# Kernel tuning notes

Hardware: AMD Instinct MI355X
Metric: run time of the kernel (lower is better)

## Reference

```python
import jax, jax.numpy as jnp
import numpy as np

N_NODES = 50000
N_EDGES = 500000
D = 256  # node_dim = edge_dim = out_dim; in_dim = 2*D


def setup_inputs() -> dict:
    key = jax.random.key(0)
    ks = jax.random.split(key, 9)
    x = jax.random.normal(ks[0], (N_NODES, D), dtype=jnp.float32)
    edge_index = jax.random.randint(ks[1], (2, N_EDGES), 0, N_NODES, dtype=jnp.int64)
    edge_attr = jax.random.normal(ks[2], (N_EDGES, D), dtype=jnp.float32)
    u = jax.random.normal(ks[3], (1, D), dtype=jnp.float32)
    batch = jnp.zeros((N_NODES,), dtype=jnp.int64)
    scale = 1.0 / np.sqrt(2 * D)
    W1 = jax.random.normal(ks[4], (2 * D, D), dtype=jnp.float32) * scale
    b1 = jax.random.normal(ks[5], (D,), dtype=jnp.float32) * scale
    W2 = jax.random.normal(ks[6], (2 * D, D), dtype=jnp.float32) * scale
    b2 = jax.random.normal(ks[7], (D,), dtype=jnp.float32) * scale
    return {"x": x, "edge_index": edge_index, "edge_attr": edge_attr, "u": u,
            "batch": batch, "W1": W1, "b1": b1, "W2": W2, "b2": b2}


def reference(x, edge_index, edge_attr, u, batch, W1, b1, W2, b2):
    row, col = edge_index[0], edge_index[1]
    # gather source-node features and concat with edge features: [E, 2D]
    h = jnp.concatenate([x[row], edge_attr], axis=1)
    h = jax.nn.relu(h @ W1 + b1)  # node_mlp_1
    # scatter-mean over destination nodes
    agg = jax.ops.segment_sum(h, col, num_segments=N_NODES)
    cnt = jax.ops.segment_sum(jnp.ones((h.shape[0],), h.dtype), col, num_segments=N_NODES)
    agg = agg / jnp.maximum(cnt, 1.0)[:, None]
    out = jnp.concatenate([x, agg], axis=1)  # [N, 2D]
    return jax.nn.relu(out @ W2 + b2)  # node_mlp_2
```

## Files before the change

kernel.cpp:

```cpp
#include <hip/hip_runtime.h>

#define N_NODES 50000
#define N_EDGES 500000
#define D 256
#define TWO_D 512

typedef __attribute__((ext_vector_type(8))) __bf16 bf16x8;
typedef __attribute__((ext_vector_type(4))) float f32x4;
typedef unsigned short ushort_t;

__device__ __forceinline__ unsigned short f2bf(float f) {
    unsigned int u = __builtin_bit_cast(unsigned int, f);
    u += 0x7FFFu + ((u >> 16) & 1u);
    return (unsigned short)(u >> 16);
}
__device__ __forceinline__ unsigned int pk2(float lo, float hi) {
    return (unsigned int)f2bf(lo) | ((unsigned int)f2bf(hi) << 16);
}


__global__ void k_zero(float* __restrict__ p, int n4) {
    int i = blockIdx.x * blockDim.x + threadIdx.x;
    if (i < n4) ((float4*)p)[i] = make_float4(0.f, 0.f, 0.f, 0.f);
}

__global__ void k_cvt_x(const float* __restrict__ x, ushort_t* __restrict__ xb, int n8) {
    int i = blockIdx.x * blockDim.x + threadIdx.x;
    if (i < n8) {
        const float4* s = (const float4*)(x + (size_t)i * 8);
        float4 a = s[0], b = s[1];
        uint4 o;
        o.x = pk2(a.x, a.y); o.y = pk2(a.z, a.w);
        o.z = pk2(b.x, b.y); o.w = pk2(b.z, b.w);
        *(uint4*)(xb + (size_t)i * 8) = o;
    }
}

__global__ void k_wt(const float* __restrict__ w, ushort_t* __restrict__ wt, int KW) {
    int n = blockIdx.x;
    for (int k = threadIdx.x; k < KW; k += blockDim.x)
        wt[(size_t)n * KW + k] = f2bf(w[(size_t)k * D + n]);
}

__global__ void k_count_i(const int* __restrict__ coli, int* __restrict__ cnt) {
    int e = blockIdx.x * blockDim.x + threadIdx.x;
    if (e < N_EDGES) atomicAdd(&cnt[coli[e]], 1);
}


__device__ __forceinline__ int iscan_block(int v, int tid) {
    int lane = tid & 63, wv = tid >> 6;
    int s = v;
    #pragma unroll
    for (int off = 1; off < 64; off <<= 1) {
        int t = __shfl_up(s, off, 64);
        if (lane >= off) s += t;
    }
    __shared__ int wsum[4];
    if (lane == 63) wsum[wv] = s;
    __syncthreads();
    #pragma unroll
    for (int w = 0; w < 3; ++w)
        if (wv > w) s += wsum[w];
    return s;
}

__global__ void k_scan_a(const int* __restrict__ cnt, int* __restrict__ rowptr,
                         int* __restrict__ bsum) {
    int i = blockIdx.x * 256 + threadIdx.x;
    int v = (i < N_NODES) ? cnt[i] : 0;
    int s = iscan_block(v, threadIdx.x);
    if (i < N_NODES) rowptr[i] = s - v;
    if (threadIdx.x == 255) bsum[blockIdx.x] = s;
}

__global__ void k_scan_b(int* __restrict__ bsum, int nb) {
    int i = threadIdx.x;
    int v = (i < nb) ? bsum[i] : 0;
    int s = iscan_block(v, i);
    if (i < nb) bsum[i] = s - v;
}

__global__ void k_scan_c(int* __restrict__ rowptr, const int* __restrict__ bsum,
                         int* __restrict__ cursor) {
    int i = blockIdx.x * 256 + threadIdx.x;
    if (i < N_NODES) {
        int r = rowptr[i] + bsum[blockIdx.x];
        rowptr[i] = r;
        cursor[i] = r;
    }
    if (i == 0) rowptr[N_NODES] = N_EDGES;
}

__global__ void k_fill(const int* __restrict__ coli, const int* __restrict__ rowi,
                       int* __restrict__ cursor, int* __restrict__ elist,
                       int* __restrict__ rowg) {
    int e = blockIdx.x * blockDim.x + threadIdx.x;
    if (e < N_EDGES) {
        int p = atomicAdd(&cursor[coli[e]], 1);
        elist[p] = e;
        rowg[p] = rowi[e];
    }
}

__global__ void k_posnode(const int* __restrict__ rowptr, int* __restrict__ posnode) {
    int p = blockIdx.x * blockDim.x + threadIdx.x;
    if (p >= N_EDGES) return;
    int lo = 0, hi = N_NODES;
    while (hi - lo > 1) {
        int mid = (lo + hi) >> 1;
        if (rowptr[mid] <= p) lo = mid; else hi = mid;
    }
    posnode[p] = lo;
}

__global__ __launch_bounds__(256) void k_xw1(
    const ushort_t* __restrict__ xb, const ushort_t* __restrict__ w1at,
    const float* __restrict__ b1, float* __restrict__ xw1)
{
    __shared__ __align__(16) ushort_t As[64 * 64];
    __shared__ __align__(16) ushort_t Bs[256 * 64];
    const int tid = threadIdx.x;
    const int wave = tid >> 6, lane = tid & 63;
    const int lr = lane & 15, lh = lane >> 4;
    const int n0 = blockIdx.x * 64;

    const int sm = tid >> 2;
    const int sc = (tid & 3) << 4;
    int ns = n0 + sm; if (ns >= N_NODES) ns = N_NODES - 1;
    const ushort_t* xrow = xb + (size_t)ns * D;
    const ushort_t* wrow = w1at + (size_t)tid * D;
    const int swA = (sm & 7) << 3;
    const int swB = (tid & 7) << 3;

    f32x4 acc[4][4];
    #pragma unroll
    for (int i = 0; i < 4; ++i)
        #pragma unroll
        for (int j = 0; j < 4; ++j)
            acc[i][j] = (f32x4){0.f, 0.f, 0.f, 0.f};

    for (int kk = 0; kk < 4; ++kk) {
        const int k0 = kk << 6;
        const uint4* sx = (const uint4*)(xrow + k0 + sc);
        uint4 av0 = sx[0], av1 = sx[1];
        const uint4* wsv = (const uint4*)(wrow + k0);
        uint4 w0 = wsv[0], w1 = wsv[1], w2 = wsv[2], w3 = wsv[3];
        uint4 w4 = wsv[4], w5 = wsv[5], w6 = wsv[6], w7 = wsv[7];

        __syncthreads();
        *(uint4*)&As[sm * 64 + ( sc      ^ swA)] = av0;
        *(uint4*)&As[sm * 64 + ((sc + 8) ^ swA)] = av1;
        {
            const int base = tid * 64;
            *(uint4*)&Bs[base + ( 0 ^ swB)] = w0;
            *(uint4*)&Bs[base + ( 8 ^ swB)] = w1;
            *(uint4*)&Bs[base + (16 ^ swB)] = w2;
            *(uint4*)&Bs[base + (24 ^ swB)] = w3;
            *(uint4*)&Bs[base + (32 ^ swB)] = w4;
            *(uint4*)&Bs[base + (40 ^ swB)] = w5;
            *(uint4*)&Bs[base + (48 ^ swB)] = w6;
            *(uint4*)&Bs[base + (56 ^ swB)] = w7;
        }
        __syncthreads();

        #pragma unroll
        for (int kh = 0; kh < 2; ++kh) {
            const int kb = kh * 32 + lh * 8;
            bf16x8 af[4], bfr[4];
            #pragma unroll
            for (int i = 0; i < 4; ++i) {
                int m = i * 16 + lr;
                af[i] = *(const bf16x8*)&As[m * 64 + (kb ^ ((m & 7) << 3))];
            }
            #pragma unroll
            for (int j = 0; j < 4; ++j) {
                int n = wave * 64 + j * 16 + lr;
                bfr[j] = *(const bf16x8*)&Bs[n * 64 + (kb ^ ((n & 7) << 3))];
            }
            #pragma unroll
            for (int i = 0; i < 4; ++i)
                #pragma unroll
                for (int j = 0; j < 4; ++j)
                    acc[i][j] = __builtin_amdgcn_mfma_f32_16x16x32_bf16(af[i], bfr[j], acc[i][j], 0, 0, 0);
        }
    }

    float bv[4];
    #pragma unroll
    for (int j = 0; j < 4; ++j) bv[j] = b1[wave * 64 + j * 16 + lr];
    #pragma unroll
    for (int i = 0; i < 4; ++i) {
        #pragma unroll
        for (int r = 0; r < 4; ++r) {
            int m = i * 16 + lh * 4 + r;
            int node = n0 + m;
            if (node < N_NODES) {
                float* orow = xw1 + (size_t)node * D;
                #pragma unroll
                for (int j = 0; j < 4; ++j)
                    orow[wave * 64 + j * 16 + lr] = acc[i][j][r] + bv[j];
            }
        }
    }
}

__global__ __launch_bounds__(256, 3) void k_edge_csr(
    const float* __restrict__ ea, const ushort_t* __restrict__ w1bt,
    const float* __restrict__ xw1, const int* __restrict__ elist,
    const int* __restrict__ rowg, const int* __restrict__ posnode,
    const int* __restrict__ rowptr, float* __restrict__ agg)
{
    __shared__ __align__(16) ushort_t As[2][64 * 64];
    __shared__ int snd[64];
    const int tid = threadIdx.x;
    const int wave = tid >> 6, lane = tid & 63;
    const int lr = lane & 15, lh = lane >> 4;
    const int p0 = blockIdx.x * 64;

    if (tid < 64) {
        int p = p0 + tid;
        snd[tid] = (p < N_EDGES) ? posnode[min(p, N_EDGES - 1)] : -1;
    }

    const int sm = tid >> 2;
    const int sc = (tid & 3) << 4;
    int ps = p0 + sm; if (ps >= N_EDGES) ps = N_EDGES - 1;
    const float* earow = ea + (size_t)elist[ps] * D;
    const int swA = (sm & 7) << 3;

    const ushort_t* pw[4];
    #pragma unroll
    for (int j = 0; j < 4; ++j)
        pw[j] = w1bt + (size_t)(wave * 64 + j * 16 + lr) * D + lh * 8;

    f32x4 acc[4][4];
    #pragma unroll
    for (int i = 0; i < 4; ++i)
        #pragma unroll
        for (int j = 0; j < 4; ++j)
            acc[i][j] = (f32x4){0.f, 0.f, 0.f, 0.f};

    float4 a0, a1, a2, a3;
    {
        const float4* s = (const float4*)(earow + sc);
        a0 = s[0]; a1 = s[1]; a2 = s[2]; a3 = s[3];
    }
    {
        uint4 av0, av1;
        av0.x = pk2(a0.x, a0.y); av0.y = pk2(a0.z, a0.w);
        av0.z = pk2(a1.x, a1.y); av0.w = pk2(a1.z, a1.w);
        av1.x = pk2(a2.x, a2.y); av1.y = pk2(a2.z, a2.w);
        av1.z = pk2(a3.x, a3.y); av1.w = pk2(a3.z, a3.w);
        *(uint4*)&As[0][sm * 64 + ( sc      ^ swA)] = av0;
        *(uint4*)&As[0][sm * 64 + ((sc + 8) ^ swA)] = av1;
    }
    {
        const float4* s = (const float4*)(earow + 64 + sc);
        a0 = s[0]; a1 = s[1]; a2 = s[2]; a3 = s[3];
    }
    __syncthreads();

    #pragma unroll
    for (int kk = 0; kk < 4; ++kk) {
        const int k0 = kk << 6;
        const ushort_t* cur = As[kk & 1];

        bf16x8 b0[4], b1[4];
        #pragma unroll
        for (int j = 0; j < 4; ++j) {
            b0[j] = *(const bf16x8*)(pw[j] + k0);
            b1[j] = *(const bf16x8*)(pw[j] + k0 + 32);
        }
        bf16x8 af0[4], af1[4];
        #pragma unroll
        for (int i = 0; i < 4; ++i) {
            const int m = i * 16 + lr;
            const int sw = (m & 7) << 3;
            af0[i] = *(const bf16x8*)&cur[m * 64 + (( lh * 8      ) ^ sw)];
            af1[i] = *(const bf16x8*)&cur[m * 64 + ((32 + lh * 8) ^ sw)];
        }
        #pragma unroll
        for (int i = 0; i < 4; ++i)
            #pragma unroll
            for (int j = 0; j < 4; ++j) {
                acc[i][j] = __builtin_amdgcn_mfma_f32_16x16x32_bf16(af0[i], b0[j], acc[i][j], 0, 0, 0);
                acc[i][j] = __builtin_amdgcn_mfma_f32_16x16x32_bf16(af1[i], b1[j], acc[i][j], 0, 0, 0);
            }

        if (kk < 3) {
            uint4 av0, av1;
            av0.x = pk2(a0.x, a0.y); av0.y = pk2(a0.z, a0.w);
            av0.z = pk2(a1.x, a1.y); av0.w = pk2(a1.z, a1.w);
            av1.x = pk2(a2.x, a2.y); av1.y = pk2(a2.z, a2.w);
            av1.z = pk2(a3.x, a3.y); av1.w = pk2(a3.z, a3.w);
            ushort_t* nxt = (ushort_t*)As[(kk + 1) & 1];
            *(uint4*)&nxt[sm * 64 + ( sc      ^ swA)] = av0;
            *(uint4*)&nxt[sm * 64 + ((sc + 8) ^ swA)] = av1;
            if (kk < 2) {
                const float4* s = (const float4*)(earow + ((kk + 2) << 6) + sc);
                a0 = s[0]; a1 = s[1]; a2 = s[2]; a3 = s[3];
            }
            __syncthreads();
        }
    }

    #pragma unroll
    for (int i = 0; i < 4; ++i) {
        #pragma unroll
        for (int r = 0; r < 4; ++r) {
            const int m = i * 16 + lh * 4 + r;
            const bool ok = (p0 + m < N_EDGES);
            const int srw = rowg[min(p0 + m, N_EDGES - 1)];
            const float* xr = xw1 + (size_t)srw * D + wave * 64 + lr;
            #pragma unroll
            for (int j = 0; j < 4; ++j) {
                float v = acc[i][j][r] + xr[j * 16];
                v = v > 0.f ? v : 0.f;
                acc[i][j][r] = ok ? v : 0.f;
            }
        }
    }

    int a = 0;
    while (a < 64) {
        const int node = snd[a];
        int b = a + 1;
        while (b < 64 && snd[b] == node) ++b;
        if (node >= 0) {
            float s0 = 0.f, s1 = 0.f, s2 = 0.f, s3 = 0.f;
            #pragma unroll
            for (int i = 0; i < 4; ++i) {
                if (b <= i * 16 || a >= (i + 1) * 16) continue;
                #pragma unroll
                for (int r = 0; r < 4; ++r) {
                    const int m = i * 16 + lh * 4 + r;
                    const bool in = (m >= a) && (m < b);
                    s0 += in ? acc[i][0][r] : 0.f;
                    s1 += in ? acc[i][1][r] : 0.f;
                    s2 += in ? acc[i][2][r] : 0.f;
                    s3 += in ? acc[i][3][r] : 0.f;
                }
            }
            s0 += __shfl_xor(s0, 16, 64); s0 += __shfl_xor(s0, 32, 64);
            s1 += __shfl_xor(s1, 16, 64); s1 += __shfl_xor(s1, 32, 64);
            s2 += __shfl_xor(s2, 16, 64); s2 += __shfl_xor(s2, 32, 64);
            s3 += __shfl_xor(s3, 16, 64); s3 += __shfl_xor(s3, 32, 64);
            if (lh == 0) {
                const bool interior = (rowptr[node] >= p0) && (rowptr[node + 1] <= p0 + 64);
                float* dst = agg + (size_t)node * D + wave * 64 + lr;
                if (interior) {
                    dst[0]  = s0; dst[16] = s1; dst[32] = s2; dst[48] = s3;
                } else {
                    atomicAdd(&dst[0],  s0); atomicAdd(&dst[16], s1);
                    atomicAdd(&dst[32], s2); atomicAdd(&dst[48], s3);
                }
            }
        }
        a = b;
    }
}

__global__ __launch_bounds__(256) void k_node(
    const ushort_t* __restrict__ xb, const float* __restrict__ agg,
    const int* __restrict__ cnti,
    const ushort_t* __restrict__ w2t, const float* __restrict__ b2,
    float* __restrict__ out)
{
    __shared__ __align__(16) ushort_t As[64 * 64];
    __shared__ __align__(16) ushort_t Bs[256 * 64];
    const int tid = threadIdx.x;
    const int wave = tid >> 6, lane = tid & 63;
    const int lr = lane & 15, lh = lane >> 4;
    const int n0 = blockIdx.x * 64;

    const int sm = tid >> 2;
    const int sc = (tid & 3) << 4;
    int ns = n0 + sm; if (ns >= N_NODES) ns = N_NODES - 1;
    const ushort_t* xrow = xb + (size_t)ns * D;
    const float*    arow = agg + (size_t)ns * D;
    const float     ic   = 1.0f / fmaxf((float)cnti[ns], 1.0f);
    const ushort_t* wrow = w2t + (size_t)tid * TWO_D;
    const int swA = (sm & 7) << 3;
    const int swB = (tid & 7) << 3;

    f32x4 acc[4][4];
    #pragma unroll
    for (int i = 0; i < 4; ++i)
        #pragma unroll
        for (int j = 0; j < 4; ++j)
            acc[i][j] = (f32x4){0.f, 0.f, 0.f, 0.f};

    for (int kk = 0; kk < 8; ++kk) {
        const int k0 = kk << 6;
        uint4 av0, av1;
        if (kk < 4) {
            const uint4* s = (const uint4*)(xrow + k0 + sc);
            av0 = s[0]; av1 = s[1];
        } else {
            const float4* s = (const float4*)(arow + (k0 - D) + sc);
            float4 f0 = s[0], f1 = s[1], f2 = s[2], f3 = s[3];
            f0.x *= ic; f0.y *= ic; f0.z *= ic; f0.w *= ic;
            f1.x *= ic; f1.y *= ic; f1.z *= ic; f1.w *= ic;
            f2.x *= ic; f2.y *= ic; f2.z *= ic; f2.w *= ic;
            f3.x *= ic; f3.y *= ic; f3.z *= ic; f3.w *= ic;
            av0.x = pk2(f0.x, f0.y); av0.y = pk2(f0.z, f0.w);
            av0.z = pk2(f1.x, f1.y); av0.w = pk2(f1.z, f1.w);
            av1.x = pk2(f2.x, f2.y); av1.y = pk2(f2.z, f2.w);
            av1.z = pk2(f3.x, f3.y); av1.w = pk2(f3.z, f3.w);
        }
        const uint4* wsv = (const uint4*)(wrow + k0);
        uint4 w0 = wsv[0], w1 = wsv[1], w2 = wsv[2], w3 = wsv[3];
        uint4 w4 = wsv[4], w5 = wsv[5], w6 = wsv[6], w7 = wsv[7];

        __syncthreads();
        *(uint4*)&As[sm * 64 + ( sc      ^ swA)] = av0;
        *(uint4*)&As[sm * 64 + ((sc + 8) ^ swA)] = av1;
        {
            const int base = tid * 64;
            *(uint4*)&Bs[base + ( 0 ^ swB)] = w0;
            *(uint4*)&Bs[base + ( 8 ^ swB)] = w1;
            *(uint4*)&Bs[base + (16 ^ swB)] = w2;
            *(uint4*)&Bs[base + (24 ^ swB)] = w3;
            *(uint4*)&Bs[base + (32 ^ swB)] = w4;
            *(uint4*)&Bs[base + (40 ^ swB)] = w5;
            *(uint4*)&Bs[base + (48 ^ swB)] = w6;
            *(uint4*)&Bs[base + (56 ^ swB)] = w7;
        }
        __syncthreads();

        #pragma unroll
        for (int kh = 0; kh < 2; ++kh) {
            const int kb = kh * 32 + lh * 8;
            bf16x8 af[4], bfr[4];
            #pragma unroll
            for (int i = 0; i < 4; ++i) {
                int m = i * 16 + lr;
                af[i] = *(const bf16x8*)&As[m * 64 + (kb ^ ((m & 7) << 3))];
            }
            #pragma unroll
            for (int j = 0; j < 4; ++j) {
                int n = wave * 64 + j * 16 + lr;
                bfr[j] = *(const bf16x8*)&Bs[n * 64 + (kb ^ ((n & 7) << 3))];
            }
            #pragma unroll
            for (int i = 0; i < 4; ++i)
                #pragma unroll
                for (int j = 0; j < 4; ++j)
                    acc[i][j] = __builtin_amdgcn_mfma_f32_16x16x32_bf16(af[i], bfr[j], acc[i][j], 0, 0, 0);
        }
    }

    float bv[4];
    #pragma unroll
    for (int j = 0; j < 4; ++j) bv[j] = b2[wave * 64 + j * 16 + lr];
    #pragma unroll
    for (int i = 0; i < 4; ++i) {
        #pragma unroll
        for (int r = 0; r < 4; ++r) {
            int m = i * 16 + lh * 4 + r;
            int node = n0 + m;
            if (node < N_NODES) {
                float* orow = out + (size_t)node * D;
                #pragma unroll
                for (int j = 0; j < 4; ++j) {
                    float v = acc[i][j][r] + bv[j];
                    orow[wave * 64 + j * 16 + lr] = v > 0.f ? v : 0.f;
                }
            }
        }
    }
}


extern "C" void kernel_launch(void* const* d_in, const int* in_sizes, int n_in,
                              void* d_out, int out_size, void* d_ws, size_t ws_size,
                              hipStream_t stream)
{
    const float* x  = (const float*)d_in[0];
    const int*   ei = (const int*)d_in[1];
    const float* ea = (const float*)d_in[2];
    const float* W1 = (const float*)d_in[5];
    const float* b1 = (const float*)d_in[6];
    const float* W2 = (const float*)d_in[7];
    const float* b2 = (const float*)d_in[8];
    float* out = (float*)d_out;

    const int* rowi = ei;
    const int* coli = ei + N_EDGES;
    char* ws = (char*)d_ws;

    size_t off = 0;
    auto take = [&](size_t bytes) {
        char* p = ws + off;
        off = (off + bytes + 255) & ~(size_t)255;
        return p;
    };

    ushort_t* xb      = (ushort_t*)take((size_t)N_NODES * D * 2);
    ushort_t* w1at    = (ushort_t*)take((size_t)D * D * 2);
    ushort_t* w1bt    = (ushort_t*)take((size_t)D * D * 2);
    ushort_t* w2t     = (ushort_t*)take((size_t)D * TWO_D * 2);
    float*    xw1     = (float*)take((size_t)N_NODES * D * 4);
    float*    agg     = (float*)take((size_t)N_NODES * D * 4);
    int*      cnti    = (int*)take(50016 * 4);
    int*      rowptr  = (int*)take(50016 * 4);
    int*      cursor  = (int*)take(50016 * 4);
    int*      bsum    = (int*)take(256 * 4);
    int*      elist   = (int*)take((size_t)N_EDGES * 4);
    int*      rowg    = (int*)take((size_t)N_EDGES * 4);
    int*      posnode = (int*)take((size_t)N_EDGES * 4);

    const int NB = (N_NODES + 255) / 256;
    const int EB = (N_EDGES + 255) / 256;
    const int NGB = (N_NODES + 63) / 64;
    const int EGB = (N_EDGES + 63) / 64;

    k_cvt_x<<<(N_NODES * D / 8 + 255) / 256, 256, 0, stream>>>(x, xb, N_NODES * D / 8);
    k_wt   <<<D, 256, 0, stream>>>(W1, w1at, D);
    k_wt   <<<D, 256, 0, stream>>>(W1 + (size_t)D * D, w1bt, D);
    k_wt   <<<D, 256, 0, stream>>>(W2, w2t, TWO_D);

    k_zero   <<<49, 256, 0, stream>>>((float*)cnti, 50016 / 4);
    k_count_i<<<EB, 256, 0, stream>>>(coli, cnti);
    k_scan_a <<<NB, 256, 0, stream>>>(cnti, rowptr, bsum);
    k_scan_b <<<1, 256, 0, stream>>>(bsum, NB);
    k_scan_c <<<NB, 256, 0, stream>>>(rowptr, bsum, cursor);
    k_fill   <<<EB, 256, 0, stream>>>(coli, rowi, cursor, elist, rowg);
    k_posnode<<<EB, 256, 0, stream>>>(rowptr, posnode);

    k_xw1    <<<NGB, 256, 0, stream>>>(xb, w1at, b1, xw1);
    k_zero   <<<(N_NODES * D / 4 + 255) / 256, 256, 0, stream>>>(agg, N_NODES * D / 4);
    k_edge_csr<<<EGB, 256, 0, stream>>>(ea, w1bt, xw1, elist, rowg, posnode, rowptr, agg);
    k_node   <<<NGB, 256, 0, stream>>>(xb, agg, cnti, w2t, b2, out);
}
```

Baseline: 477.2 us.

## Process edges in natural order, write bf16 h to CSR slots, aggregate separately

The edge GEMM now reads edge_attr rows contiguously in natural order instead of gathering through a CSR edge list, then scatters the bf16 relu output into its CSR slot in a new per-edge buffer. A separate k_agg kernel computes the segment mean per node, and the node GEMM reads bf16 aggregates directly. The xw1 intermediate becomes bf16, and the posnode binary search and the agg zeroing are dropped. The cost is an extra 256 MB bf16 h write and read, plus some bf16 rounding of intermediates.

```diff
diff --git a/kernel.cpp b/kernel.cpp
--- a/kernel.cpp
+++ b/kernel.cpp
@@ -16,6 +16,9 @@
 }
 __device__ __forceinline__ unsigned int pk2(float lo, float hi) {
     return (unsigned int)f2bf(lo) | ((unsigned int)f2bf(hi) << 16);
+}
+__device__ __forceinline__ float bf2f(ushort_t u) {
+    return __builtin_bit_cast(float, ((unsigned int)u) << 16);
 }
 
 
@@ -92,31 +95,16 @@
     if (i == 0) rowptr[N_NODES] = N_EDGES;
 }
 
-__global__ void k_fill(const int* __restrict__ coli, const int* __restrict__ rowi,
-                       int* __restrict__ cursor, int* __restrict__ elist,
-                       int* __restrict__ rowg) {
+__global__ void k_fill_pos(const int* __restrict__ coli, int* __restrict__ cursor,
+                           int* __restrict__ csrpos) {
     int e = blockIdx.x * blockDim.x + threadIdx.x;
-    if (e < N_EDGES) {
-        int p = atomicAdd(&cursor[coli[e]], 1);
-        elist[p] = e;
-        rowg[p] = rowi[e];
-    }
-}
-
-__global__ void k_posnode(const int* __restrict__ rowptr, int* __restrict__ posnode) {
-    int p = blockIdx.x * blockDim.x + threadIdx.x;
-    if (p >= N_EDGES) return;
-    int lo = 0, hi = N_NODES;
-    while (hi - lo > 1) {
-        int mid = (lo + hi) >> 1;
-        if (rowptr[mid] <= p) lo = mid; else hi = mid;
-    }
-    posnode[p] = lo;
+    if (e < N_EDGES)
+        csrpos[e] = atomicAdd(&cursor[coli[e]], 1);
 }
 
 __global__ __launch_bounds__(256) void k_xw1(
     const ushort_t* __restrict__ xb, const ushort_t* __restrict__ w1at,
-    const float* __restrict__ b1, float* __restrict__ xw1)
+    const float* __restrict__ b1, ushort_t* __restrict__ xw1b)
 {
     __shared__ __align__(16) ushort_t As[64 * 64];
     __shared__ __align__(16) ushort_t Bs[256 * 64];
@@ -196,37 +184,30 @@
             int m = i * 16 + lh * 4 + r;
             int node = n0 + m;
             if (node < N_NODES) {
-                float* orow = xw1 + (size_t)node * D;
+                ushort_t* orow = xw1b + (size_t)node * D + wave * 64 + lr;
                 #pragma unroll
                 for (int j = 0; j < 4; ++j)
-                    orow[wave * 64 + j * 16 + lr] = acc[i][j][r] + bv[j];
-            }
-        }
-    }
-}
-
-__global__ __launch_bounds__(256, 3) void k_edge_csr(
+                    orow[j * 16] = f2bf(acc[i][j][r] + bv[j]);
+            }
+        }
+    }
+}
+
+__global__ __launch_bounds__(256, 3) void k_edge_nat(
     const float* __restrict__ ea, const ushort_t* __restrict__ w1bt,
-    const float* __restrict__ xw1, const int* __restrict__ elist,
-    const int* __restrict__ rowg, const int* __restrict__ posnode,
-    const int* __restrict__ rowptr, float* __restrict__ agg)
+    const ushort_t* __restrict__ xw1b, const int* __restrict__ rowi,
+    const int* __restrict__ csrpos, ushort_t* __restrict__ h)
 {
     __shared__ __align__(16) ushort_t As[2][64 * 64];
-    __shared__ int snd[64];
     const int tid = threadIdx.x;
     const int wave = tid >> 6, lane = tid & 63;
     const int lr = lane & 15, lh = lane >> 4;
-    const int p0 = blockIdx.x * 64;
-
-    if (tid < 64) {
-        int p = p0 + tid;
-        snd[tid] = (p < N_EDGES) ? posnode[min(p, N_EDGES - 1)] : -1;
-    }
+    const int e0 = blockIdx.x * 64;
 
     const int sm = tid >> 2;
     const int sc = (tid & 3) << 4;
-    int ps = p0 + sm; if (ps >= N_EDGES) ps = N_EDGES - 1;
-    const float* earow = ea + (size_t)elist[ps] * D;
+    int es = e0 + sm; if (es >= N_EDGES) es = N_EDGES - 1;
+    const float* earow = ea + (size_t)es * D;
     const int swA = (sm & 7) << 3;
 
     const ushort_t* pw[4];
@@ -277,7 +258,7 @@
         for (int i = 0; i < 4; ++i) {
             const int m = i * 16 + lr;
             const int sw = (m & 7) << 3;
-            af0[i] = *(const bf16x8*)&cur[m * 64 + (( lh * 8      ) ^ sw)];
+            af0[i] = *(const bf16x8*)&cur[m * 64 + (( lh * 8     ) ^ sw)];
             af1[i] = *(const bf16x8*)&cur[m * 64 + ((32 + lh * 8) ^ sw)];
         }
         #pragma unroll
@@ -310,60 +291,45 @@
         #pragma unroll
         for (int r = 0; r < 4; ++r) {
             const int m = i * 16 + lh * 4 + r;
-            const bool ok = (p0 + m < N_EDGES);
-            const int srw = rowg[min(p0 + m, N_EDGES - 1)];
-            const float* xr = xw1 + (size_t)srw * D + wave * 64 + lr;
-            #pragma unroll
-            for (int j = 0; j < 4; ++j) {
-                float v = acc[i][j][r] + xr[j * 16];
-                v = v > 0.f ? v : 0.f;
-                acc[i][j][r] = ok ? v : 0.f;
-            }
-        }
-    }
-
-    int a = 0;
-    while (a < 64) {
-        const int node = snd[a];
-        int b = a + 1;
-        while (b < 64 && snd[b] == node) ++b;
-        if (node >= 0) {
-            float s0 = 0.f, s1 = 0.f, s2 = 0.f, s3 = 0.f;
-            #pragma unroll
-            for (int i = 0; i < 4; ++i) {
-                if (b <= i * 16 || a >= (i + 1) * 16) continue;
+            const int e = e0 + m;
+            if (e < N_EDGES) {
+                const int srw = rowi[e];
+                const ushort_t* xr = xw1b + (size_t)srw * D + wave * 64 + lr;
+                const int p = csrpos[e];
+                ushort_t* hrow = h + (size_t)p * D + wave * 64 + lr;
                 #pragma unroll
-                for (int r = 0; r < 4; ++r) {
-                    const int m = i * 16 + lh * 4 + r;
-                    const bool in = (m >= a) && (m < b);
-                    s0 += in ? acc[i][0][r] : 0.f;
-                    s1 += in ? acc[i][1][r] : 0.f;
-                    s2 += in ? acc[i][2][r] : 0.f;
-                    s3 += in ? acc[i][3][r] : 0.f;
+                for (int j = 0; j < 4; ++j) {
+                    float v = acc[i][j][r] + bf2f(xr[j * 16]);
+                    hrow[j * 16] = f2bf(v > 0.f ? v : 0.f);
                 }
             }
-            s0 += __shfl_xor(s0, 16, 64); s0 += __shfl_xor(s0, 32, 64);
-            s1 += __shfl_xor(s1, 16, 64); s1 += __shfl_xor(s1, 32, 64);
-            s2 += __shfl_xor(s2, 16, 64); s2 += __shfl_xor(s2, 32, 64);
-            s3 += __shfl_xor(s3, 16, 64); s3 += __shfl_xor(s3, 32, 64);
-            if (lh == 0) {
-                const bool interior = (rowptr[node] >= p0) && (rowptr[node + 1] <= p0 + 64);
-                float* dst = agg + (size_t)node * D + wave * 64 + lr;
-                if (interior) {
-                    dst[0]  = s0; dst[16] = s1; dst[32] = s2; dst[48] = s3;
-                } else {
-                    atomicAdd(&dst[0],  s0); atomicAdd(&dst[16], s1);
-                    atomicAdd(&dst[32], s2); atomicAdd(&dst[48], s3);
-                }
-            }
-        }
-        a = b;
-    }
+        }
+    }
+}
+
+__global__ __launch_bounds__(256) void k_agg(
+    const ushort_t* __restrict__ h, const int* __restrict__ rowptr,
+    ushort_t* __restrict__ aggb)
+{
+    int node = blockIdx.x * 4 + (threadIdx.x >> 6);
+    if (node >= N_NODES) return;
+    int lane = threadIdx.x & 63;
+    int beg = rowptr[node], end = rowptr[node + 1];
+    float a0 = 0.f, a1 = 0.f, a2 = 0.f, a3 = 0.f;
+    const ushort_t* hp = h + (size_t)beg * D + lane * 4;
+    for (int it = 0; it < end - beg; ++it) {
+        ushort4 u = *(const ushort4*)(hp + (size_t)it * D);
+        a0 += bf2f(u.x); a1 += bf2f(u.y); a2 += bf2f(u.z); a3 += bf2f(u.w);
+    }
+    float inv = 1.0f / fmaxf((float)(end - beg), 1.0f);
+    ushort4 o;
+    o.x = f2bf(a0 * inv); o.y = f2bf(a1 * inv);
+    o.z = f2bf(a2 * inv); o.w = f2bf(a3 * inv);
+    *(ushort4*)(aggb + (size_t)node * D + lane * 4) = o;
 }
 
 __global__ __launch_bounds__(256) void k_node(
-    const ushort_t* __restrict__ xb, const float* __restrict__ agg,
-    const int* __restrict__ cnti,
+    const ushort_t* __restrict__ xb, const ushort_t* __restrict__ aggb,
     const ushort_t* __restrict__ w2t, const float* __restrict__ b2,
     float* __restrict__ out)
 {
@@ -377,10 +343,9 @@
     const int sm = tid >> 2;
     const int sc = (tid & 3) << 4;
     int ns = n0 + sm; if (ns >= N_NODES) ns = N_NODES - 1;
-    const ushort_t* xrow = xb + (size_t)ns * D;
-    const float*    arow = agg + (size_t)ns * D;
-    const float     ic   = 1.0f / fmaxf((float)cnti[ns], 1.0f);
-    const ushort_t* wrow = w2t + (size_t)tid * TWO_D;
+    const ushort_t* xrow = xb   + (size_t)ns * D;
+    const ushort_t* arow = aggb + (size_t)ns * D;
+    const ushort_t* wrow = w2t  + (size_t)tid * TWO_D;
     const int swA = (sm & 7) << 3;
     const int swB = (tid & 7) << 3;
 
@@ -398,16 +363,8 @@
             const uint4* s = (const uint4*)(xrow + k0 + sc);
             av0 = s[0]; av1 = s[1];
         } else {
-            const float4* s = (const float4*)(arow + (k0 - D) + sc);
-            float4 f0 = s[0], f1 = s[1], f2 = s[2], f3 = s[3];
-            f0.x *= ic; f0.y *= ic; f0.z *= ic; f0.w *= ic;
-            f1.x *= ic; f1.y *= ic; f1.z *= ic; f1.w *= ic;
-            f2.x *= ic; f2.y *= ic; f2.z *= ic; f2.w *= ic;
-            f3.x *= ic; f3.y *= ic; f3.z *= ic; f3.w *= ic;
-            av0.x = pk2(f0.x, f0.y); av0.y = pk2(f0.z, f0.w);
-            av0.z = pk2(f1.x, f1.y); av0.w = pk2(f1.z, f1.w);
-            av1.x = pk2(f2.x, f2.y); av1.y = pk2(f2.z, f2.w);
-            av1.z = pk2(f3.x, f3.y); av1.w = pk2(f3.z, f3.w);
+            const uint4* s = (const uint4*)(arow + (k0 - D) + sc);
+            av0 = s[0]; av1 = s[1];
         }
         const uint4* wsv = (const uint4*)(wrow + k0);
         uint4 w0 = wsv[0], w1 = wsv[1], w2 = wsv[2], w3 = wsv[3];
@@ -501,15 +458,14 @@
     ushort_t* w1at    = (ushort_t*)take((size_t)D * D * 2);
     ushort_t* w1bt    = (ushort_t*)take((size_t)D * D * 2);
     ushort_t* w2t     = (ushort_t*)take((size_t)D * TWO_D * 2);
-    float*    xw1     = (float*)take((size_t)N_NODES * D * 4);
-    float*    agg     = (float*)take((size_t)N_NODES * D * 4);
+    ushort_t* xw1b    = (ushort_t*)take((size_t)N_NODES * D * 2);
+    ushort_t* h       = (ushort_t*)take((size_t)N_EDGES * D * 2);
     int*      cnti    = (int*)take(50016 * 4);
     int*      rowptr  = (int*)take(50016 * 4);
     int*      cursor  = (int*)take(50016 * 4);
     int*      bsum    = (int*)take(256 * 4);
-    int*      elist   = (int*)take((size_t)N_EDGES * 4);
-    int*      rowg    = (int*)take((size_t)N_EDGES * 4);
-    int*      posnode = (int*)take((size_t)N_EDGES * 4);
+    int*      csrpos  = (int*)take((size_t)N_EDGES * 4);
+    ushort_t* aggb    = xw1b;
 
     const int NB = (N_NODES + 255) / 256;
     const int EB = (N_EDGES + 255) / 256;
@@ -521,16 +477,15 @@
     k_wt   <<<D, 256, 0, stream>>>(W1 + (size_t)D * D, w1bt, D);
     k_wt   <<<D, 256, 0, stream>>>(W2, w2t, TWO_D);
 
-    k_zero   <<<49, 256, 0, stream>>>((float*)cnti, 50016 / 4);
-    k_count_i<<<EB, 256, 0, stream>>>(coli, cnti);
-    k_scan_a <<<NB, 256, 0, stream>>>(cnti, rowptr, bsum);
-    k_scan_b <<<1, 256, 0, stream>>>(bsum, NB);
-    k_scan_c <<<NB, 256, 0, stream>>>(rowptr, bsum, cursor);
-    k_fill   <<<EB, 256, 0, stream>>>(coli, rowi, cursor, elist, rowg);
-    k_posnode<<<EB, 256, 0, stream>>>(rowptr, posnode);
-
-    k_xw1    <<<NGB, 256, 0, stream>>>(xb, w1at, b1, xw1);
-    k_zero   <<<(N_NODES * D / 4 + 255) / 256, 256, 0, stream>>>(agg, N_NODES * D / 4);
-    k_edge_csr<<<EGB, 256, 0, stream>>>(ea, w1bt, xw1, elist, rowg, posnode, rowptr, agg);
-    k_node   <<<NGB, 256, 0, stream>>>(xb, agg, cnti, w2t, b2, out);
-}
+    k_zero    <<<49, 256, 0, stream>>>((float*)cnti, 50016 / 4);
+    k_count_i <<<EB, 256, 0, stream>>>(coli, cnti);
+    k_scan_a  <<<NB, 256, 0, stream>>>(cnti, rowptr, bsum);
+    k_scan_b  <<<1, 256, 0, stream>>>(bsum, NB);
+    k_scan_c  <<<NB, 256, 0, stream>>>(rowptr, bsum, cursor);
+    k_fill_pos<<<EB, 256, 0, stream>>>(coli, cursor, csrpos);
+
+    k_xw1     <<<NGB, 256, 0, stream>>>(xb, w1at, b1, xw1b);
+    k_edge_nat<<<EGB, 256, 0, stream>>>(ea, w1bt, xw1b, rowi, csrpos, h);
+    k_agg     <<<(N_NODES + 3) / 4, 256, 0, stream>>>(h, rowptr, aggb);
+    k_node    <<<NGB, 256, 0, stream>>>(xb, aggb, w2t, b2, out);
+}
```

Result: slower. 522.5 us (+9.5%).
